# Optimization experiments

Hardware: AMD Instinct MI355X
Metric: run time of the kernel (lower is better)

The kernel has to match this reference:

```python
import jax, jax.numpy as jnp
import numpy as np

N, NFEAT, NHID, NREL, NCLASS, NHEADS = 4096, 512, 64, 64, 16, 8
ALPHA = 0.2   # LeakyReLU negative slope
NEG = -9e15   # pyGAT mask value


def _gat_layer(x, rel, mask, adj_ad, W, a1, a2, concat):
    # x: [N, Fin], rel: [nrel, Fin], mask: [N, N] bool, adj_ad: [N, nrel]
    xr = x + adj_ad @ rel                 # relation-augmented node features
    h = xr @ W                            # [N, Fout]
    f1 = h @ a1                           # [N]  (a^T[Wh_i||Wh_j] = f1_i + f2_j)
    f2 = h @ a2                           # [N]
    e = jax.nn.leaky_relu(f1[:, None] + f2[None, :], ALPHA)  # [N, N]
    att = jax.nn.softmax(jnp.where(mask, e, NEG), axis=1)
    out = att @ h                         # [N, Fout]
    return jax.nn.elu(out) if concat else out


def setup_inputs() -> dict:
    key = jax.random.key(0)
    ks = jax.random.split(key, 12)
    x = jax.random.normal(ks[0], (N, NFEAT), jnp.float32)
    rel = jax.random.normal(ks[1], (NREL, NFEAT), jnp.float32)
    rel_dict = jax.random.randint(ks[2], (N,), 0, NREL, jnp.int32)
    adj = (jax.random.uniform(ks[3], (N, N)) < 0.01).astype(jnp.float32)
    adj = jnp.maximum(adj, jnp.eye(N, dtype=jnp.float32))  # self loops
    adj_ad = jax.random.uniform(ks[4], (N, NREL), jnp.float32)
    adj_ad = adj_ad / adj_ad.sum(axis=1, keepdims=True)
    s_in = 1.0 / np.sqrt(NFEAT)
    s_hid = 1.0 / np.sqrt(NHID)
    s_cat = 1.0 / np.sqrt(NHID * NHEADS)
    W_heads = jax.random.normal(ks[5], (NHEADS, NFEAT, NHID), jnp.float32) * s_in
    a1_heads = jax.random.normal(ks[6], (NHEADS, NHID), jnp.float32) * s_hid
    a2_heads = jax.random.normal(ks[7], (NHEADS, NHID), jnp.float32) * s_hid
    W_out = jax.random.normal(ks[8], (NHID * NHEADS, NFEAT), jnp.float32) * s_cat
    a1_out = jax.random.normal(ks[9], (NFEAT,), jnp.float32) * s_in
    a2_out = jax.random.normal(ks[10], (NFEAT,), jnp.float32) * s_in
    lin_W = jax.random.normal(ks[11], (NFEAT, NCLASS), jnp.float32) * s_in
    lin_b = jnp.zeros((NCLASS,), jnp.float32)
    return {"x": x, "rel": rel, "rel_dict": rel_dict, "adj": adj, "adj_ad": adj_ad,
            "W_heads": W_heads, "a1_heads": a1_heads, "a2_heads": a2_heads,
            "W_out": W_out, "a1_out": a1_out, "a2_out": a2_out,
            "lin_W": lin_W, "lin_b": lin_b}


def reference(x, rel, rel_dict, adj, adj_ad, W_heads, a1_heads, a2_heads,
              W_out, a1_out, a2_out, lin_W, lin_b):
    # dropout is identity at inference (training=False); rel_dict is only used
    # by the repo to build adj/adj_ad, so it is a non-math constant here.
    mask = adj > 0
    # multi-head GAT layer, heads fused via vmap then concatenated on feature dim
    heads = jax.vmap(lambda W, a1, a2: _gat_layer(x, rel, mask, adj_ad, W, a1, a2, True))(
        W_heads, a1_heads, a2_heads)                      # [H, N, NHID]
    hcat = jnp.moveaxis(heads, 0, 1).reshape(N, NHEADS * NHID)  # [N, H*NHID]
    h2 = _gat_layer(hcat, rel, mask, adj_ad, W_out, a1_out, a2_out, False)  # [N, NFEAT]
    logits = jax.nn.elu(h2 @ lin_W + lin_b)               # [N, NCLASS]
    return jax.nn.log_softmax(logits, axis=1)
```

## Files before the change

### kernel.cpp

```cpp
#include <hip/hip_runtime.h>

#define NN      4096
#define FEAT    512
#define KDIM    576
#define NHID    64
#define NHEADS  8
#define NCLS    16
#define MAXDEG  128
#define ALPHA   0.2f

typedef __bf16 bf16_t;
typedef __bf16 bf16x8_t __attribute__((ext_vector_type(8)));
typedef float  f32x4_t  __attribute__((ext_vector_type(4)));
typedef unsigned short us8_t __attribute__((ext_vector_type(8)));

__device__ inline unsigned short f2bf(float f) {
    unsigned int u = __float_as_uint(f);
    u += 0x7fffu + ((u >> 16) & 1u);
    return (unsigned short)(u >> 16);
}
__device__ inline float bfu2f(unsigned short b) {
    return __uint_as_float(((unsigned int)b) << 16);
}
__device__ inline void gload16(const void* g, void* s) {
    __builtin_amdgcn_global_load_lds(
        (const __attribute__((address_space(1))) void*)g,
        (__attribute__((address_space(3))) void*)s, 16, 0, 0);
}

#define PREP_REL0   0
#define PREP_TR0    256
#define PREP_Z0     384
#define PREP_CAST0  456
#define PREP_CSR0   2504
#define PREP_NBLK   3528

__global__ __launch_bounds__(256) void prep_kernel(
    const float* __restrict__ adj, int* __restrict__ deg, int* __restrict__ cols,
    const float* __restrict__ adj_ad, const float* __restrict__ rel,
    const float* __restrict__ x, bf16_t* __restrict__ Abf,
    bf16_t* __restrict__ Abf2,
    const float* __restrict__ Wh, const float* __restrict__ Wo,
    unsigned short* __restrict__ WcT, unsigned short* __restrict__ WoT,
    float* __restrict__ fzero) {
    int b = blockIdx.x;
    int t = threadIdx.x;
    __shared__ float smem[64 * 65];
    if (b < PREP_TR0) {
        int r  = b & 63;
        int nh = (b >> 6) & 1;
        int n  = nh * 256 + t;
        smem[t]       = rel[r * FEAT + t];
        smem[t + 256] = rel[r * FEAT + 256 + t];
        __syncthreads();
        float acc[8] = {};
        if (b < 128) {
            int h = n >> 6, f = n & 63;
            const float* p = Wh + (size_t)h * 32768 + f;
            for (int k0 = 0; k0 < 512; k0 += 8)
                #pragma unroll
                for (int u = 0; u < 8; ++u)
                    acc[u] += smem[k0 + u] * p[(size_t)(k0 + u) * 64];
            float s = ((acc[0] + acc[1]) + (acc[2] + acc[3]))
                    + ((acc[4] + acc[5]) + (acc[6] + acc[7]));
            WcT[(size_t)n * KDIM + 512 + r] = f2bf(s);
        } else {
            const float* p = Wo + n;
            for (int k0 = 0; k0 < 512; k0 += 8)
                #pragma unroll
                for (int u = 0; u < 8; ++u)
                    acc[u] += smem[k0 + u] * p[(size_t)(k0 + u) * 512];
            float s = ((acc[0] + acc[1]) + (acc[2] + acc[3]))
                    + ((acc[4] + acc[5]) + (acc[6] + acc[7]));
            WoT[(size_t)n * KDIM + 512 + r] = f2bf(s);
        }
    } else if (b < PREP_Z0) {
        int tb = b - PREP_TR0;
        if (tb < 64) {
            int h = tb >> 3, k0 = (tb & 7) * 64;
            const float* src = Wh + (size_t)h * 32768 + (size_t)k0 * 64;
            #pragma unroll
            for (int i2 = 0; i2 < 16; ++i2) {
                int li = t + i2 * 256;
                float v = src[li];
                smem[(li & 63) * 65 + (li >> 6)] = v;
            }
            __syncthreads();
            #pragma unroll
            for (int i2 = 0; i2 < 16; ++i2) {
                int li = t + i2 * 256;
                int f = li >> 6, r = li & 63;
                WcT[(size_t)(h * 64 + f) * KDIM + k0 + r] = f2bf(smem[f * 65 + r]);
            }
        } else {
            int wb = tb - 64;
            int n0 = (wb & 7) * 64, k0 = (wb >> 3) * 64;
            #pragma unroll
            for (int i2 = 0; i2 < 16; ++i2) {
                int li = t + i2 * 256;
                int r = li >> 6, f = li & 63;
                float v = Wo[(size_t)(k0 + r) * 512 + n0 + f];
                smem[f * 65 + r] = v;
            }
            __syncthreads();
            #pragma unroll
            for (int i2 = 0; i2 < 16; ++i2) {
                int li = t + i2 * 256;
                int f = li >> 6, r = li & 63;
                WoT[(size_t)(n0 + f) * KDIM + k0 + r] = f2bf(smem[f * 65 + r]);
            }
        }
    } else if (b < PREP_CAST0) {
        int g = (b - PREP_Z0) * 256 + t;
        ((float4*)fzero)[g] = make_float4(0.f, 0.f, 0.f, 0.f);
    } else if (b < PREP_CSR0) {
        int half = t >> 7;
        int tt = t & 127;
        size_t i = (size_t)(b - PREP_CAST0) * 2 + half;
        float4 xv = ((const float4*)(x + i * FEAT))[tt];
        ushort4 o;
        o.x = f2bf(xv.x); o.y = f2bf(xv.y);
        o.z = f2bf(xv.z); o.w = f2bf(xv.w);
        *(ushort4*)(Abf + i * KDIM + 4 * tt) = o;
        if (tt < 16) {
            float4 av = ((const float4*)(adj_ad + i * 64))[tt];
            ushort4 o2;
            o2.x = f2bf(av.x); o2.y = f2bf(av.y);
            o2.z = f2bf(av.z); o2.w = f2bf(av.w);
            *(ushort4*)(Abf  + i * KDIM + 512 + 4 * tt) = o2;
            *(ushort4*)(Abf2 + i * KDIM + 512 + 4 * tt) = o2;
        }
    } else {
        int l = t & 63;
        int i = (b - PREP_CSR0) * 4 + (t >> 6);
        const float4* row4 = (const float4*)(adj + (size_t)i * NN);
        float4 v[16];
        #pragma unroll
        for (int c2 = 0; c2 < 16; ++c2) v[c2] = row4[l + c2 * 64];
        unsigned long long mask = 0;
        #pragma unroll
        for (int c2 = 0; c2 < 16; ++c2) {
            unsigned m4 = (unsigned)(v[c2].x > 0.0f)
                        | ((unsigned)(v[c2].y > 0.0f) << 1)
                        | ((unsigned)(v[c2].z > 0.0f) << 2)
                        | ((unsigned)(v[c2].w > 0.0f) << 3);
            mask |= (unsigned long long)m4 << (4 * c2);
        }
        int c = __popcll(mask);
        int pre = c;
        #pragma unroll
        for (int off = 1; off < 64; off <<= 1) {
            int n = __shfl_up(pre, off);
            if (l >= off) pre += n;
        }
        int base = pre - c;
        if (l == 63) deg[i] = pre > MAXDEG ? MAXDEG : pre;
        int* colrow = cols + i * MAXDEG;
        int idx = base;
        while (mask) {
            int bit = (int)__ffsll(mask) - 1;
            mask &= mask - 1;
            int j = 4 * l + ((bit >> 2) << 8) + (bit & 3);
            if (idx < MAXDEG) colrow[idx] = j;
            ++idx;
        }
    }
}

__global__ __launch_bounds__(256) void gemm_bf16_dot_kernel(
    const bf16_t* __restrict__ A, const bf16_t* __restrict__ Bt,
    unsigned short* __restrict__ Cbf,
    const float* __restrict__ a1, const float* __restrict__ a2,
    float* __restrict__ f1, float* __restrict__ f2, int layer2) {
    __shared__ __align__(16) bf16_t As[64][64];
    __shared__ __align__(16) bf16_t Bs[64][64];
    const int bm = blockIdx.x * 64;
    const int bn = blockIdx.y * 64;
    const int by = blockIdx.y;
    const int t  = threadIdx.x;
    const int l  = t & 63;
    const int w  = t >> 6;
    const int wr = w >> 1;
    const int wc = w & 1;
    const int c16 = l & 15;
    const int q8  = (l >> 4) * 8;
    const int r4  = (l >> 4) * 4;

    const bf16_t* Abase = A  + (size_t)bm * KDIM;
    const bf16_t* Bbase = Bt + (size_t)bn * KDIM;

    f32x4_t acc[2][2] = {};
    for (int k0 = 0; k0 < KDIM; k0 += 64) {
        #pragma unroll
        for (int c = 0; c < 2; ++c) {
            int cb = c * 256 + w * 64;
            int li = cb + l;
            int r = li >> 3, pc = li & 7;
            int lc = pc ^ (r & 7);
            gload16(Abase + (size_t)r * KDIM + k0 + lc * 8,
                    (char*)&As[0][0] + cb * 16);
        }
        #pragma unroll
        for (int c = 0; c < 2; ++c) {
            int cb = c * 256 + w * 64;
            int li = cb + l;
            int r = li >> 3, pc = li & 7;
            int lc = pc ^ (r & 7);
            gload16(Bbase + (size_t)r * KDIM + k0 + lc * 8,
                    (char*)&Bs[0][0] + cb * 16);
        }
        __syncthreads();
        #pragma unroll
        for (int kk = 0; kk < 64; kk += 32) {
            const int ck = (kk + q8) >> 3;
            bf16x8_t af[2], bfr[2];
            #pragma unroll
            for (int mi = 0; mi < 2; ++mi) {
                int R = wr * 32 + mi * 16 + c16;
                af[mi] = *(const bf16x8_t*)&As[R][(ck ^ (R & 7)) * 8];
            }
            #pragma unroll
            for (int ni = 0; ni < 2; ++ni) {
                int R = wc * 32 + ni * 16 + c16;
                bfr[ni] = *(const bf16x8_t*)&Bs[R][(ck ^ (R & 7)) * 8];
            }
            #pragma unroll
            for (int mi = 0; mi < 2; ++mi)
                #pragma unroll
                for (int ni = 0; ni < 2; ++ni)
                    acc[mi][ni] = __builtin_amdgcn_mfma_f32_16x16x32_bf16(
                        af[mi], bfr[ni], acc[mi][ni], 0, 0, 0);
        }
        __syncthreads();
    }
    #pragma unroll
    for (int mi = 0; mi < 2; ++mi)
        #pragma unroll
        for (int ni = 0; ni < 2; ++ni)
            #pragma unroll
            for (int r = 0; r < 4; ++r)
                Cbf[(size_t)(bm + wr * 32 + mi * 16 + r4 + r) * FEAT
                    + bn + wc * 32 + ni * 16 + c16] = f2bf(acc[mi][ni][r]);

    float a1v[2], a2v[2];
    #pragma unroll
    for (int ni = 0; ni < 2; ++ni) {
        a1v[ni] = a1[bn + wc * 32 + ni * 16 + c16];
        a2v[ni] = a2[bn + wc * 32 + ni * 16 + c16];
    }
    float p1[2][4] = {}, p2[2][4] = {};
    #pragma unroll
    for (int mi = 0; mi < 2; ++mi)
        #pragma unroll
        for (int ni = 0; ni < 2; ++ni)
            #pragma unroll
            for (int r = 0; r < 4; ++r) {
                p1[mi][r] += acc[mi][ni][r] * a1v[ni];
                p2[mi][r] += acc[mi][ni][r] * a2v[ni];
            }
    #pragma unroll
    for (int off = 1; off <= 8; off <<= 1)
        #pragma unroll
        for (int mi = 0; mi < 2; ++mi)
            #pragma unroll
            for (int r = 0; r < 4; ++r) {
                p1[mi][r] += __shfl_xor(p1[mi][r], off);
                p2[mi][r] += __shfl_xor(p2[mi][r], off);
            }
    if (c16 == 0) {
        int fbase = layer2 ? 0 : by * NN;
        #pragma unroll
        for (int mi = 0; mi < 2; ++mi)
            #pragma unroll
            for (int r = 0; r < 4; ++r) {
                int row = bm + wr * 32 + mi * 16 + r4 + r;
                atomicAdd(&f1[fbase + row], p1[mi][r]);
                atomicAdd(&f2[fbase + row], p2[mi][r]);
            }
    }
}

__global__ __launch_bounds__(512) void att1_kernel(
    const bf16_t* __restrict__ Hbf, const float* __restrict__ f1,
    const float* __restrict__ f2, const int* __restrict__ deg,
    const int* __restrict__ cols, bf16_t* __restrict__ outbf) {
    int i = blockIdx.x;
    int tid = threadIdx.x;
    int h = tid >> 6;
    int l = tid & 63;
    __shared__ int jl[MAXDEG];
    __shared__ float se[NHEADS][MAXDEG];
    __shared__ float part[NHEADS][FEAT];
    __shared__ float sinv[NHEADS];
    __shared__ int sdeg;
    if (tid == 0) sdeg = deg[i];
    __syncthreads();
    int d = sdeg;
    int dpad = (d + 31) & ~31;
    for (int k = tid; k < dpad; k += 512)
        jl[k] = (k < d) ? cols[i * MAXDEG + k] : i;
    __syncthreads();
    float fi = f1[h * NN + i];
    float lmax = -1e30f;
    for (int k = l; k < d; k += 64) {
        float e = fi + f2[h * NN + jl[k]];
        e = e > 0.0f ? e : ALPHA * e;
        se[h][k] = e;
        lmax = fmaxf(lmax, e);
    }
    for (int off = 32; off; off >>= 1) lmax = fmaxf(lmax, __shfl_down(lmax, off));
    float m = __shfl(lmax, 0);
    float ls = 0.0f;
    for (int k = l; k < d; k += 64) {
        float p = __expf(se[h][k] - m);
        se[h][k] = p;
        ls += p;
    }
    for (int k = d + l; k < dpad; k += 64) se[h][k] = 0.0f;
    for (int off = 32; off; off >>= 1) ls += __shfl_down(ls, off);
    if (l == 0) sinv[h] = 1.0f / ls;
    __syncthreads();
    const int myhead = l >> 3;
    float acc[8] = {};
    for (int k0 = 0; k0 < dpad; k0 += 32) {
        float pw[4];
        const bf16_t* rp[4];
        #pragma unroll
        for (int j = 0; j < 4; ++j) {
            int k = k0 + j * 8 + h;
            pw[j] = se[myhead][k];
            rp[j] = Hbf + (size_t)jl[k] * FEAT + l * 8;
        }
        #pragma unroll
        for (int j = 0; j < 4; ++j) {
            us8_t v = *(const us8_t*)rp[j];
            float p = pw[j];
            #pragma unroll
            for (int q = 0; q < 8; ++q) acc[q] += p * bfu2f(v[q]);
        }
    }
    *(float4*)&part[h][l * 8]     = make_float4(acc[0], acc[1], acc[2], acc[3]);
    *(float4*)&part[h][l * 8 + 4] = make_float4(acc[4], acc[5], acc[6], acc[7]);
    __syncthreads();
    {
        float sum = 0.0f;
        #pragma unroll
        for (int w2 = 0; w2 < NHEADS; ++w2) sum += part[w2][tid];
        float o = sum * sinv[tid >> 6];
        o = o > 0.0f ? o : __expf(o) - 1.0f;
        ((unsigned short*)outbf)[(size_t)i * KDIM + tid] = f2bf(o);
    }
}

__global__ __launch_bounds__(256) void att2_final_kernel(
    const bf16_t* __restrict__ Hbf, const float* __restrict__ f1,
    const float* __restrict__ f2, const int* __restrict__ deg,
    const int* __restrict__ cols, const float* __restrict__ linW,
    const float* __restrict__ linb, float* __restrict__ out) {
    int i = blockIdx.x;
    int t = threadIdx.x;
    __shared__ int jl[MAXDEG];
    __shared__ float sp[MAXDEG];
    __shared__ float red[4];
    __shared__ float part[3][FEAT];
    __shared__ float hrow[FEAT];
    __shared__ float clsred[16][NCLS];
    __shared__ float sl[NCLS];
    __shared__ int sdeg;
    if (t == 0) sdeg = deg[i];
    __syncthreads();
    int d = sdeg;
    int dpad = (d + 15) & ~15;
    if (t < dpad) jl[t] = (t < d) ? cols[i * MAXDEG + t] : i;
    __syncthreads();
    float e = 0.0f, lmax = -1e30f;
    if (t < d) {
        e = f1[i] + f2[jl[t]];
        e = e > 0.0f ? e : ALPHA * e;
        lmax = e;
    }
    for (int off = 32; off; off >>= 1) lmax = fmaxf(lmax, __shfl_down(lmax, off));
    if ((t & 63) == 0) red[t >> 6] = lmax;
    __syncthreads();
    float m = fmaxf(fmaxf(red[0], red[1]), fmaxf(red[2], red[3]));
    float p = 0.0f;
    if (t < d) p = __expf(e - m);
    if (t < dpad) sp[t] = p;
    float ls = p;
    for (int off = 32; off; off >>= 1) ls += __shfl_down(ls, off);
    __syncthreads();
    if ((t & 63) == 0) red[t >> 6] = ls;
    __syncthreads();
    float s = red[0] + red[1] + red[2] + red[3];
    float inv = 1.0f / s;
    const int slot = t >> 6;
    const int cg   = t & 63;
    float acc[8] = {};
    for (int k0 = 0; k0 < dpad; k0 += 16) {
        float pw[4];
        const bf16_t* rp[4];
        #pragma unroll
        for (int j = 0; j < 4; ++j) {
            int k = k0 + j * 4 + slot;
            pw[j] = sp[k];
            rp[j] = Hbf + (size_t)jl[k] * FEAT + cg * 8;
        }
        #pragma unroll
        for (int j = 0; j < 4; ++j) {
            us8_t v = *(const us8_t*)rp[j];
            float pk = pw[j];
            #pragma unroll
            for (int q = 0; q < 8; ++q) acc[q] += pk * bfu2f(v[q]);
        }
    }
    if (slot > 0) {
        float* dst = &part[slot - 1][cg * 8];
        *(float4*)(dst)     = make_float4(acc[0], acc[1], acc[2], acc[3]);
        *(float4*)(dst + 4) = make_float4(acc[4], acc[5], acc[6], acc[7]);
    }
    __syncthreads();
    if (slot == 0) {
        #pragma unroll
        for (int sl2 = 0; sl2 < 3; ++sl2)
            #pragma unroll
            for (int j = 0; j < 8; ++j) acc[j] += part[sl2][cg * 8 + j];
        float* dst = &hrow[cg * 8];
        *(float4*)(dst)     = make_float4(acc[0] * inv, acc[1] * inv, acc[2] * inv, acc[3] * inv);
        *(float4*)(dst + 4) = make_float4(acc[4] * inv, acc[5] * inv, acc[6] * inv, acc[7] * inv);
    }
    __syncthreads();
    {
        int c = t & 15;
        int seg = t >> 4;
        float partial = 0.0f;
        int f0 = seg * 32;
        #pragma unroll 8
        for (int f = f0; f < f0 + 32; ++f) partial += hrow[f] * linW[f * NCLS + c];
        clsred[seg][c] = partial;
    }
    __syncthreads();
    if (t < NCLS) {
        float logit = linb[t];
        #pragma unroll
        for (int seg = 0; seg < 16; ++seg) logit += clsred[seg][t];
        logit = logit > 0.0f ? logit : __expf(logit) - 1.0f;
        sl[t] = logit;
    }
    __syncthreads();
    if (t < NCLS) {
        float mm = sl[0];
        #pragma unroll
        for (int c = 1; c < NCLS; ++c) mm = fmaxf(mm, sl[c]);
        float ssum = 0.0f;
        #pragma unroll
        for (int c = 0; c < NCLS; ++c) ssum += __expf(sl[c] - mm);
        out[i * NCLS + t] = sl[t] - mm - logf(ssum);
    }
}

extern "C" void kernel_launch(void* const* d_in, const int* in_sizes, int n_in,
                              void* d_out, int out_size, void* d_ws, size_t ws_size,
                              hipStream_t stream) {
    const float* x        = (const float*)d_in[0];
    const float* rel      = (const float*)d_in[1];
    const float* adj      = (const float*)d_in[3];
    const float* adj_ad   = (const float*)d_in[4];
    const float* W_heads  = (const float*)d_in[5];
    const float* a1_heads = (const float*)d_in[6];
    const float* a2_heads = (const float*)d_in[7];
    const float* W_out    = (const float*)d_in[8];
    const float* a1_out   = (const float*)d_in[9];
    const float* a2_out   = (const float*)d_in[10];
    const float* lin_W    = (const float*)d_in[11];
    const float* lin_b    = (const float*)d_in[12];
    float* out = (float*)d_out;

    char* ws = (char*)d_ws;
    bf16_t* Abf  = (bf16_t*)(ws);
    bf16_t* Abf2 = (bf16_t*)(ws + (5u  << 20));
    bf16_t* Hbf1 = (bf16_t*)(ws + (10u << 20));
    bf16_t* Hbf2 = (bf16_t*)(ws + (14u << 20));
    bf16_t* WcT  = (bf16_t*)(ws + (18u << 20));
    bf16_t* WoT  = (bf16_t*)(ws + (19u << 20));
    float*  f1   = (float*) (ws + (20u << 20));
    float*  f2   = (float*) (ws + (20u << 20) + (128u << 10));
    float*  f1o  = (float*) (ws + (20u << 20) + (256u << 10));
    float*  f2o  = (float*) (ws + (20u << 20) + (272u << 10));
    int*    deg  = (int*)   (ws + (20u << 20) + (288u << 10));
    int*    cols = (int*)   (ws + (21u << 20));

    prep_kernel<<<PREP_NBLK, 256, 0, stream>>>(
        adj, deg, cols, adj_ad, rel, x, Abf, Abf2, W_heads, W_out,
        (unsigned short*)WcT, (unsigned short*)WoT, f1);
    gemm_bf16_dot_kernel<<<dim3(64, 8), 256, 0, stream>>>(
        Abf, WcT, (unsigned short*)Hbf1, a1_heads, a2_heads, f1, f2, 0);
    att1_kernel<<<NN, 512, 0, stream>>>(Hbf1, f1, f2, deg, cols, Abf2);
    gemm_bf16_dot_kernel<<<dim3(64, 8), 256, 0, stream>>>(
        Abf2, WoT, (unsigned short*)Hbf2, a1_out, a2_out, f1o, f2o, 1);
    att2_final_kernel<<<NN, 256, 0, stream>>>(Hbf2, f1o, f2o, deg, cols, lin_W, lin_b, out);
}
```

Measured before the change: 189.7 us.

## Reassociate layer-2 aggregation with linear head to aggregate 16-wide projections

```diff
diff --git a/kernel.cpp b/kernel.cpp
--- a/kernel.cpp
+++ b/kernel.cpp
@@ -31,9 +31,9 @@
 #define PREP_REL0   0
 #define PREP_TR0    256
 #define PREP_Z0     384
-#define PREP_CAST0  456
-#define PREP_CSR0   2504
-#define PREP_NBLK   3528
+#define PREP_CAST0  520
+#define PREP_CSR0   2568
+#define PREP_NBLK   3592
 
 __global__ __launch_bounds__(256) void prep_kernel(
     const float* __restrict__ adj, int* __restrict__ deg, int* __restrict__ cols,
@@ -171,9 +171,10 @@
     const bf16_t* __restrict__ A, const bf16_t* __restrict__ Bt,
     unsigned short* __restrict__ Cbf,
     const float* __restrict__ a1, const float* __restrict__ a2,
-    float* __restrict__ f1, float* __restrict__ f2, int layer2) {
-    __shared__ __align__(16) bf16_t As[64][64];
-    __shared__ __align__(16) bf16_t Bs[64][64];
+    float* __restrict__ f1, float* __restrict__ f2, int layer2,
+    const float* __restrict__ linW, float* __restrict__ G) {
+    __shared__ __align__(16) bf16_t ABs[2][64][64];
+    float* Ct = (float*)ABs;
     const int bm = blockIdx.x * 64;
     const int bn = blockIdx.y * 64;
     const int by = blockIdx.y;
@@ -198,7 +199,7 @@
             int r = li >> 3, pc = li & 7;
             int lc = pc ^ (r & 7);
             gload16(Abase + (size_t)r * KDIM + k0 + lc * 8,
-                    (char*)&As[0][0] + cb * 16);
+                    (char*)&ABs[0][0][0] + cb * 16);
         }
         #pragma unroll
         for (int c = 0; c < 2; ++c) {
@@ -207,7 +208,7 @@
             int r = li >> 3, pc = li & 7;
             int lc = pc ^ (r & 7);
             gload16(Bbase + (size_t)r * KDIM + k0 + lc * 8,
-                    (char*)&Bs[0][0] + cb * 16);
+                    (char*)&ABs[1][0][0] + cb * 16);
         }
         __syncthreads();
         #pragma unroll
@@ -217,12 +218,12 @@
             #pragma unroll
             for (int mi = 0; mi < 2; ++mi) {
                 int R = wr * 32 + mi * 16 + c16;
-                af[mi] = *(const bf16x8_t*)&As[R][(ck ^ (R & 7)) * 8];
+                af[mi] = *(const bf16x8_t*)&ABs[0][R][(ck ^ (R & 7)) * 8];
             }
             #pragma unroll
             for (int ni = 0; ni < 2; ++ni) {
                 int R = wc * 32 + ni * 16 + c16;
-                bfr[ni] = *(const bf16x8_t*)&Bs[R][(ck ^ (R & 7)) * 8];
+                bfr[ni] = *(const bf16x8_t*)&ABs[1][R][(ck ^ (R & 7)) * 8];
             }
             #pragma unroll
             for (int mi = 0; mi < 2; ++mi)
@@ -233,6 +234,16 @@
         }
         __syncthreads();
     }
+    if (layer2) {
+        #pragma unroll
+        for (int mi = 0; mi < 2; ++mi)
+            #pragma unroll
+            for (int ni = 0; ni < 2; ++ni)
+                #pragma unroll
+                for (int r = 0; r < 4; ++r)
+                    Ct[(wr * 32 + mi * 16 + r4 + r) * 64
+                       + wc * 32 + ni * 16 + c16] = acc[mi][ni][r];
+    }
     #pragma unroll
     for (int mi = 0; mi < 2; ++mi)
         #pragma unroll
@@ -277,6 +288,22 @@
                 atomicAdd(&f1[fbase + row], p1[mi][r]);
                 atomicAdd(&f2[fbase + row], p2[mi][r]);
             }
+    }
+    if (layer2) {
+        __syncthreads();
+        int row = t >> 2;
+        int cls0 = (t & 3) * 4;
+        float pg[4] = {};
+        #pragma unroll 8
+        for (int c = 0; c < 64; ++c) {
+            float cv = Ct[row * 64 + c];
+            float4 wv = *(const float4*)&linW[(size_t)(bn + c) * NCLS + cls0];
+            pg[0] += cv * wv.x; pg[1] += cv * wv.y;
+            pg[2] += cv * wv.z; pg[3] += cv * wv.w;
+        }
+        #pragma unroll
+        for (int j = 0; j < 4; ++j)
+            atomicAdd(&G[(size_t)(bm + row) * NCLS + cls0 + j], pg[j]);
     }
 }
 
@@ -353,17 +380,15 @@
 }
 
 __global__ __launch_bounds__(256) void att2_final_kernel(
-    const bf16_t* __restrict__ Hbf, const float* __restrict__ f1,
+    const float* __restrict__ G, const float* __restrict__ f1,
     const float* __restrict__ f2, const int* __restrict__ deg,
-    const int* __restrict__ cols, const float* __restrict__ linW,
-    const float* __restrict__ linb, float* __restrict__ out) {
+    const int* __restrict__ cols, const float* __restrict__ linb,
+    float* __restrict__ out) {
     int i = blockIdx.x;
     int t = threadIdx.x;
     __shared__ int jl[MAXDEG];
     __shared__ float sp[MAXDEG];
     __shared__ float red[4];
-    __shared__ float part[3][FEAT];
-    __shared__ float hrow[FEAT];
     __shared__ float clsred[16][NCLS];
     __shared__ float sl[NCLS];
     __shared__ int sdeg;
@@ -393,56 +418,20 @@
     __syncthreads();
     float s = red[0] + red[1] + red[2] + red[3];
     float inv = 1.0f / s;
-    const int slot = t >> 6;
-    const int cg   = t & 63;
-    float acc[8] = {};
-    for (int k0 = 0; k0 < dpad; k0 += 16) {
-        float pw[4];
-        const bf16_t* rp[4];
-        #pragma unroll
-        for (int j = 0; j < 4; ++j) {
-            int k = k0 + j * 4 + slot;
-            pw[j] = sp[k];
-            rp[j] = Hbf + (size_t)jl[k] * FEAT + cg * 8;
-        }
-        #pragma unroll
-        for (int j = 0; j < 4; ++j) {
-            us8_t v = *(const us8_t*)rp[j];
-            float pk = pw[j];
-            #pragma unroll
-            for (int q = 0; q < 8; ++q) acc[q] += pk * bfu2f(v[q]);
-        }
-    }
-    if (slot > 0) {
-        float* dst = &part[slot - 1][cg * 8];
-        *(float4*)(dst)     = make_float4(acc[0], acc[1], acc[2], acc[3]);
-        *(float4*)(dst + 4) = make_float4(acc[4], acc[5], acc[6], acc[7]);
-    }
-    __syncthreads();
-    if (slot == 0) {
-        #pragma unroll
-        for (int sl2 = 0; sl2 < 3; ++sl2)
-            #pragma unroll
-            for (int j = 0; j < 8; ++j) acc[j] += part[sl2][cg * 8 + j];
-        float* dst = &hrow[cg * 8];
-        *(float4*)(dst)     = make_float4(acc[0] * inv, acc[1] * inv, acc[2] * inv, acc[3] * inv);
-        *(float4*)(dst + 4) = make_float4(acc[4] * inv, acc[5] * inv, acc[6] * inv, acc[7] * inv);
-    }
-    __syncthreads();
     {
-        int c = t & 15;
-        int seg = t >> 4;
-        float partial = 0.0f;
-        int f0 = seg * 32;
-        #pragma unroll 8
-        for (int f = f0; f < f0 + 32; ++f) partial += hrow[f] * linW[f * NCLS + c];
-        clsred[seg][c] = partial;
+        int slot = t >> 4;
+        int cls  = t & 15;
+        float fa[4] = {};
+        for (int k = slot; k < dpad; k += 16)
+            fa[(k >> 4) & 3] += sp[k] * G[(size_t)jl[k] * NCLS + cls];
+        clsred[slot][cls] = (fa[0] + fa[1]) + (fa[2] + fa[3]);
     }
     __syncthreads();
     if (t < NCLS) {
-        float logit = linb[t];
-        #pragma unroll
-        for (int seg = 0; seg < 16; ++seg) logit += clsred[seg][t];
+        float dot = 0.0f;
+        #pragma unroll
+        for (int seg = 0; seg < 16; ++seg) dot += clsred[seg][t];
+        float logit = linb[t] + dot * inv;
         logit = logit > 0.0f ? logit : __expf(logit) - 1.0f;
         sl[t] = logit;
     }
@@ -486,16 +475,19 @@
     float*  f2   = (float*) (ws + (20u << 20) + (128u << 10));
     float*  f1o  = (float*) (ws + (20u << 20) + (256u << 10));
     float*  f2o  = (float*) (ws + (20u << 20) + (272u << 10));
-    int*    deg  = (int*)   (ws + (20u << 20) + (288u << 10));
+    float*  G    = (float*) (ws + (20u << 20) + (288u << 10));
+    int*    deg  = (int*)   (ws + (20u << 20) + (544u << 10));
     int*    cols = (int*)   (ws + (21u << 20));
 
     prep_kernel<<<PREP_NBLK, 256, 0, stream>>>(
         adj, deg, cols, adj_ad, rel, x, Abf, Abf2, W_heads, W_out,
         (unsigned short*)WcT, (unsigned short*)WoT, f1);
     gemm_bf16_dot_kernel<<<dim3(64, 8), 256, 0, stream>>>(
-        Abf, WcT, (unsigned short*)Hbf1, a1_heads, a2_heads, f1, f2, 0);
+        Abf, WcT, (unsigned short*)Hbf1, a1_heads, a2_heads, f1, f2, 0,
+        nullptr, nullptr);
     att1_kernel<<<NN, 512, 0, stream>>>(Hbf1, f1, f2, deg, cols, Abf2);
     gemm_bf16_dot_kernel<<<dim3(64, 8), 256, 0, stream>>>(
-        Abf2, WoT, (unsigned short*)Hbf2, a1_out, a2_out, f1o, f2o, 1);
-    att2_final_kernel<<<NN, 256, 0, stream>>>(Hbf2, f1o, f2o, deg, cols, lin_W, lin_b, out);
-}
+        Abf2, WoT, (unsigned short*)Hbf2, a1_out, a2_out, f1o, f2o, 1,
+        lin_W, G);
+    att2_final_kernel<<<NN, 256, 0, stream>>>(G, f1o, f2o, deg, cols, lin_b, out);
+}
```

New measurement: 188.3 us. Within noise of the previous version (-0.7%).
